# Performance work log

Hardware: AMD Instinct MI355X
Metric: run time of the kernel (lower is better)

Reference implementation:

```python
import jax, jax.numpy as jnp
import numpy as np

H = 8
DQ = 32
DK = 32
DV = 32
DC = DQ + DK  # concat dim for additive attention


def setup_inputs() -> dict:
    key = jax.random.key(0)
    ks = jax.random.split(key, 8)
    bs, Lq, Lk = 2, 384, 384
    q = jax.random.normal(ks[0], (bs, Lq, H * DQ), jnp.float32)
    k = jax.random.normal(ks[1], (bs, Lk, H * DK), jnp.float32)
    v = jax.random.normal(ks[2], (bs, Lk, H * DV), jnp.float32)
    q_sequence_lengths = jax.random.randint(ks[3], (bs,), 1, Lq + 1, dtype=jnp.int32)
    k_sequence_lengths = jax.random.randint(ks[4], (bs,), 1, Lk + 1, dtype=jnp.int32)
    bound = 1.0 / np.sqrt(DC)
    w1 = jax.random.uniform(ks[5], (H, DC, DC), jnp.float32, -bound, bound)
    b1 = jax.random.uniform(ks[6], (H, DC), jnp.float32, -bound, bound)
    w2 = jax.random.uniform(ks[7], (H, DC), jnp.float32, -1.0, 1.0)
    return {"q": q, "k": k, "v": v,
            "q_sequence_lengths": q_sequence_lengths,
            "k_sequence_lengths": k_sequence_lengths,
            "w1": w1, "b1": b1, "w2": w2}


def reference(q, k, v, q_sequence_lengths, k_sequence_lengths, w1, b1, w2):
    bs, Lq, _ = q.shape
    Lk = k.shape[1]
    # split heads: (b, h, L, d)
    qh = q.reshape(bs, Lq, H, DQ).transpose(0, 2, 1, 3)
    kh = k.reshape(bs, Lk, H, DK).transpose(0, 2, 1, 3)
    vh = v.reshape(bs, Lk, H, DV).transpose(0, 2, 1, 3)
    # additive scores: tanh(cat(q_i, k_j) @ W1 + b1) @ w2
    # cat @ W1 == q @ W1[:DQ] + k @ W1[DQ:]  (avoids materializing the cat)
    qW = jnp.einsum('bhqd,hde->bhqe', qh, w1[:, :DQ, :])
    kW = jnp.einsum('bhkd,hde->bhke', kh, w1[:, DQ:, :])
    hid = jnp.tanh(qW[:, :, :, None, :] + kW[:, :, None, :, :] + b1[None, :, None, None, :])  # (b,h,q,k,DC)
    scores = jnp.einsum('bhqke,he->bhqk', hid, w2)
    # key-side length mask (end padded)
    kmask = jnp.arange(Lk)[None, :] < k_sequence_lengths[:, None]  # (b, Lk)
    scores = jnp.where(kmask[:, None, None, :], scores, jnp.float32(-1e9))
    att = jax.nn.softmax(scores, axis=-1)  # (b,h,q,k)
    out = jnp.einsum('bhqk,bhkd->bqhd', att, vh)  # (b,q,h,DV)
    # query-side length mask zeros out padded query rows
    qmask = jnp.arange(Lq)[None, :] < q_sequence_lengths[:, None]  # (b, Lq)
    out = out * qmask[:, :, None, None].astype(out.dtype)
    return out.reshape(bs, Lq, H * DV), att
```

## Files before the change

kernel.cpp:

```cpp
#include <hip/hip_runtime.h>

#define NH 8
#define LQ 384
#define LK 384
#define BS 2

typedef float v4f __attribute__((ext_vector_type(4)));
__device__ __forceinline__ v4f fma4(v4f a, v4f b, v4f c) { return __builtin_elementwise_fma(a, b, c); }
__device__ __forceinline__ v4f sp4(float x) { v4f r; r.x = x; r.y = x; r.z = x; r.w = x; return r; }

__global__ __launch_bounds__(256) void pre_ek_kernel(
    const float* __restrict__ kin, const float* __restrict__ w1,
    const float* __restrict__ b1, float* __restrict__ ws)
{
    __shared__ float tile[16][65];
    const int bid = blockIdx.x;
    const int bh = bid / 24, kt = bid % 24;
    const int b = bh >> 3, h = bh & 7;
    const int k0 = kt * 16;
    const int tid = threadIdx.x;
    const int lane = tid & 63, w = tid >> 6;

    float w1c[32];
    const float* w1p = w1 + (size_t)(h * 64 + 32) * 64 + lane;
    #pragma unroll
    for (int d = 0; d < 32; ++d) w1c[d] = w1p[d * 64];
    const float bv = b1[h * 64 + lane];

    #pragma unroll
    for (int s = 0; s < 4; ++s) {
        int kr = w * 4 + s;
        const float* krow = kin + ((size_t)(b * LK + k0 + kr)) * (NH * 32) + h * 32;
        float acc = bv;
        #pragma unroll
        for (int d = 0; d < 32; ++d) acc = __builtin_fmaf(krow[d], w1c[d], acc);
        tile[kr][lane] = __expf(acc + acc);
    }
    __syncthreads();
    {
        int e4 = tid >> 4, k16 = tid & 15;
        float4 o;
        o.x = tile[k16][e4 * 4 + 0];
        o.y = tile[k16][e4 * 4 + 1];
        o.z = tile[k16][e4 * 4 + 2];
        o.w = tile[k16][e4 * 4 + 3];
        ((float4*)ws)[((size_t)(bh * 16 + e4)) * LK + k0 + k16] = o;
    }
}

__global__ __launch_bounds__(256) void attn_kernel(
    const float* __restrict__ qin, const float* __restrict__ vin,
    const int* __restrict__ qlens, const int* __restrict__ klens,
    const float* __restrict__ w1, const float* __restrict__ w2g,
    const float* __restrict__ ws,
    float* __restrict__ outg, float* __restrict__ attg)
{
    __shared__ __align__(16) float eqi_s[2][256];
    __shared__ __align__(16) float att_h[4][4 * 192];
    __shared__ __align__(16) float w2s[64];
    __shared__ float2 smu[2][4][2];
    __shared__ __align__(16) float4 pvp[2][2][4][8];

    const int tid = threadIdx.x, wave = tid >> 6, lane = tid & 63;
    const int pair = wave >> 1, hh = wave & 1;
    const int bh = blockIdx.x / 48, tile = blockIdx.x % 48;
    const int b = bh >> 3, h = bh & 7;
    const int q0 = tile * 8;
    const int klen = klens[b], qlen = qlens[b];

    {
        float w1c[32];
        const float* w1p = w1 + (size_t)h * 64 * 64 + lane;
        #pragma unroll
        for (int d = 0; d < 32; ++d) w1c[d] = w1p[d * 64];
        #pragma unroll
        for (int j = 0; j < 2; ++j) {
            int r = wave * 2 + j;
            const float* qp = qin + ((size_t)(b * LQ + q0 + r)) * (NH * 32) + h * 32;
            float a = 0.f;
            #pragma unroll
            for (int d = 0; d < 32; ++d) a = __builtin_fmaf(qp[d], w1c[d], a);
            eqi_s[r >> 2][lane * 4 + (r & 3)] = __expf(a + a);
        }
        if (wave == 0) w2s[lane] = w2g[h * 64 + lane];
    }
    __syncthreads();

    v4f sc[3];
    sc[0] = sp4(0.f); sc[1] = sp4(0.f); sc[2] = sp4(0.f);
    const float4* ekq = (const float4*)ws + ((size_t)bh * 16) * LK + hh * 192 + lane;
    const v4f*   eqp = (const v4f*)eqi_s[pair];
    const float4* w2p = (const float4*)w2s;

    float4 kva[3], kvb[3];
    #pragma unroll
    for (int c = 0; c < 3; ++c) kva[c] = ekq[c * 64];
    #pragma unroll
    for (int c = 0; c < 3; ++c) kvb[c] = ekq[LK + c * 64];

    #pragma unroll
    for (int e4 = 0; e4 < 16; ++e4) {
        float4* cur = (e4 & 1) ? kvb : kva;
        float4 kq0 = cur[0], kq1 = cur[1], kq2 = cur[2];
        if (e4 < 14) {
            const float4* np = ekq + (size_t)(e4 + 2) * LK;
            cur[0] = np[0]; cur[1] = np[64]; cur[2] = np[128];
        }
        v4f E0 = eqp[e4 * 4 + 0];
        v4f E1 = eqp[e4 * 4 + 1];
        v4f E2 = eqp[e4 * 4 + 2];
        v4f E3 = eqp[e4 * 4 + 3];
        float4 wv = w2p[e4];
        float4 kqs[3] = {kq0, kq1, kq2};
        #pragma unroll
        for (int c = 0; c < 3; ++c) {
            float4 kq = kqs[c];
            v4f t0 = fma4(E0, sp4(kq.x), sp4(1.f));
            v4f t1 = fma4(E1, sp4(kq.y), sp4(1.f));
            v4f t2 = fma4(E2, sp4(kq.z), sp4(1.f));
            v4f t3 = fma4(E3, sp4(kq.w), sp4(1.f));
            v4f p12 = t0 * t1, p34 = t2 * t3;
            v4f n12 = fma4(sp4(wv.y), t0, sp4(wv.x) * t1);
            v4f n34 = fma4(sp4(wv.w), t2, sp4(wv.z) * t3);
            v4f num = fma4(n34, p12, n12 * p34);
            v4f den = p12 * p34;
            v4f r;
            r.x = __builtin_amdgcn_rcpf(den.x);
            r.y = __builtin_amdgcn_rcpf(den.y);
            r.z = __builtin_amdgcn_rcpf(den.z);
            r.w = __builtin_amdgcn_rcpf(den.w);
            sc[c] = fma4(num, r, sc[c]);
        }
    }

    float s_[3][4];
    float m_[4] = {-3.4e38f, -3.4e38f, -3.4e38f, -3.4e38f};
    #pragma unroll
    for (int c = 0; c < 3; ++c) {
        int kk = hh * 192 + c * 64 + lane;
        bool ok = kk < klen;
        #pragma unroll
        for (int r = 0; r < 4; ++r) {
            s_[c][r] = ok ? -2.0f * sc[c][r] : -3.4e38f;
            m_[r] = fmaxf(m_[r], s_[c][r]);
        }
    }
    #pragma unroll
    for (int off = 32; off >= 1; off >>= 1) {
        #pragma unroll
        for (int r = 0; r < 4; ++r) m_[r] = fmaxf(m_[r], __shfl_xor(m_[r], off));
    }
    float e_[3][4];
    float u_[4] = {0.f, 0.f, 0.f, 0.f};
    #pragma unroll
    for (int c = 0; c < 3; ++c) {
        int kk = hh * 192 + c * 64 + lane;
        bool ok = kk < klen;
        #pragma unroll
        for (int r = 0; r < 4; ++r) {
            e_[c][r] = ok ? __expf(s_[c][r] - m_[r]) : 0.f;
            u_[r] += e_[c][r];
        }
    }
    #pragma unroll
    for (int off = 32; off >= 1; off >>= 1) {
        #pragma unroll
        for (int r = 0; r < 4; ++r) u_[r] += __shfl_xor(u_[r], off);
    }
    if (lane == 0) {
        #pragma unroll
        for (int r = 0; r < 4; ++r) smu[pair][r][hh] = make_float2(m_[r], u_[r]);
    }
    {
        float* ar = att_h[wave];
        #pragma unroll
        for (int c = 0; c < 3; ++c)
            #pragma unroll
            for (int r = 0; r < 4; ++r)
                ar[r * 192 + c * 64 + lane] = e_[c][r];
    }

    const int kf = lane >> 3, dg = lane & 7;
    const float* vbase = vin + (size_t)b * LK * (NH * 32) + h * 32
                       + (size_t)(hh * 192 + kf) * (NH * 32) + dg * 4;
    const float* ap = att_h[wave];
    float oa[4][4] = {{0.f,0.f,0.f,0.f},{0.f,0.f,0.f,0.f},{0.f,0.f,0.f,0.f},{0.f,0.f,0.f,0.f}};
    float4 vbuf[2];
    vbuf[0] = *(const float4*)(vbase);
    vbuf[1] = *(const float4*)(vbase + (size_t)8 * (NH * 32));
    #pragma unroll
    for (int i = 0; i < 24; ++i) {
        float4 vv = vbuf[i & 1];
        if (i < 22) vbuf[i & 1] = *(const float4*)(vbase + (size_t)((i + 2) * 8) * (NH * 32));
        int k0 = i * 8;
        #pragma unroll
        for (int r = 0; r < 4; ++r) {
            float a = ap[r * 192 + k0 + kf];
            oa[r][0] = __builtin_fmaf(a, vv.x, oa[r][0]);
            oa[r][1] = __builtin_fmaf(a, vv.y, oa[r][1]);
            oa[r][2] = __builtin_fmaf(a, vv.z, oa[r][2]);
            oa[r][3] = __builtin_fmaf(a, vv.w, oa[r][3]);
        }
    }
    #pragma unroll
    for (int r = 0; r < 4; ++r)
        #pragma unroll
        for (int u = 0; u < 4; ++u) {
            oa[r][u] += __shfl_xor(oa[r][u], 8);
            oa[r][u] += __shfl_xor(oa[r][u], 16);
            oa[r][u] += __shfl_xor(oa[r][u], 32);
        }
    __syncthreads();

    float f_[4];
    #pragma unroll
    for (int r = 0; r < 4; ++r) {
        float2 A = smu[pair][r][0], B = smu[pair][r][1];
        float mm = fmaxf(A.x, B.x);
        float uu = A.y * __expf(A.x - mm) + B.y * __expf(B.x - mm);
        f_[r] = __expf(m_[r] - mm) * __builtin_amdgcn_rcpf(uu);
    }

    if (kf == 0) {
        #pragma unroll
        for (int r = 0; r < 4; ++r)
            pvp[pair][hh][r][dg] = make_float4(oa[r][0] * f_[r], oa[r][1] * f_[r],
                                               oa[r][2] * f_[r], oa[r][3] * f_[r]);
    }
    __syncthreads();

    if (lane < 16) {
        int r = wave * 2 + (lane >> 3);
        int dgo = lane & 7;
        int q = q0 + r;
        float4 xa = pvp[r >> 2][0][r & 3][dgo];
        float4 xb = pvp[r >> 2][1][r & 3][dgo];
        float4 o4;
        bool ok = (q < qlen);
        o4.x = ok ? (xa.x + xb.x) : 0.f;
        o4.y = ok ? (xa.y + xb.y) : 0.f;
        o4.z = ok ? (xa.z + xb.z) : 0.f;
        o4.w = ok ? (xa.w + xb.w) : 0.f;
        ((float4*)(outg + ((size_t)(b * LQ + q)) * (NH * 32) + h * 32))[dgo] = o4;
    }

    {
        float* ag = attg + ((size_t)(bh * LQ + q0 + pair * 4)) * LK + hh * 192;
        #pragma unroll
        for (int r = 0; r < 4; ++r) {
            #pragma unroll
            for (int c = 0; c < 3; ++c) ag[c * 64 + lane] = e_[c][r] * f_[r];
            ag += LK;
        }
    }
}

extern "C" void kernel_launch(void* const* d_in, const int* in_sizes, int n_in,
                              void* d_out, int out_size, void* d_ws, size_t ws_size,
                              hipStream_t stream) {
    const float* q    = (const float*)d_in[0];
    const float* k    = (const float*)d_in[1];
    const float* v    = (const float*)d_in[2];
    const int*   qlen = (const int*)d_in[3];
    const int*   klen = (const int*)d_in[4];
    const float* w1   = (const float*)d_in[5];
    const float* b1   = (const float*)d_in[6];
    const float* w2   = (const float*)d_in[7];
    float* out = (float*)d_out;
    float* att = out + (size_t)BS * LQ * NH * 32;
    float* ws  = (float*)d_ws;

    pre_ek_kernel<<<384, 256, 0, stream>>>(k, w1, b1, ws);
    attn_kernel<<<768, 256, 0, stream>>>(q, v, qlen, klen, w1, w2, ws, out, att);
}
```

Measured before the change: 94.54 us.

## Repartition attention block to six waves each owning 64 keys for all 8 queries

The attention kernel moves from 4 waves (2 query groups × 2 key halves of 192) to 6 waves, each handling 64 keys for all 8 query rows with 8-wide vector math. Each ws key-feature load is now reused across 8 queries instead of 4, which cuts global reads of the precomputed key exponentials and shortens the per-thread serial loop. Softmax statistics and partial PV results are combined across 6 waves through shared memory, and the attention writes move before the final barrier. The cost is more threads per block, more registers for 8-row accumulators, and a heavier cross-wave reduction.

```diff
diff --git a/kernel.cpp b/kernel.cpp
--- a/kernel.cpp
+++ b/kernel.cpp
@@ -5,9 +5,9 @@
 #define LK 384
 #define BS 2
 
-typedef float v4f __attribute__((ext_vector_type(4)));
-__device__ __forceinline__ v4f fma4(v4f a, v4f b, v4f c) { return __builtin_elementwise_fma(a, b, c); }
-__device__ __forceinline__ v4f sp4(float x) { v4f r; r.x = x; r.y = x; r.z = x; r.w = x; return r; }
+typedef float v8f __attribute__((ext_vector_type(8)));
+__device__ __forceinline__ v8f fma8(v8f a, v8f b, v8f c) { return __builtin_elementwise_fma(a, b, c); }
+__device__ __forceinline__ v8f sp8(float x) { v8f r = {x, x, x, x, x, x, x, x}; return r; }
 
 __global__ __launch_bounds__(256) void pre_ek_kernel(
     const float* __restrict__ kin, const float* __restrict__ w1,
@@ -48,27 +48,26 @@
     }
 }
 
-__global__ __launch_bounds__(256) void attn_kernel(
+__global__ __launch_bounds__(384) void attn_kernel(
     const float* __restrict__ qin, const float* __restrict__ vin,
     const int* __restrict__ qlens, const int* __restrict__ klens,
     const float* __restrict__ w1, const float* __restrict__ w2g,
     const float* __restrict__ ws,
     float* __restrict__ outg, float* __restrict__ attg)
 {
-    __shared__ __align__(16) float eqi_s[2][256];
-    __shared__ __align__(16) float att_h[4][4 * 192];
+    __shared__ __align__(32) float eqi_s[8 * 64];
+    __shared__ __align__(16) float att_h[6][512];
     __shared__ __align__(16) float w2s[64];
-    __shared__ float2 smu[2][4][2];
-    __shared__ __align__(16) float4 pvp[2][2][4][8];
+    __shared__ float2 smu[6][8];
+    __shared__ __align__(16) float4 pvp[6][8][8];
 
     const int tid = threadIdx.x, wave = tid >> 6, lane = tid & 63;
-    const int pair = wave >> 1, hh = wave & 1;
     const int bh = blockIdx.x / 48, tile = blockIdx.x % 48;
     const int b = bh >> 3, h = bh & 7;
     const int q0 = tile * 8;
     const int klen = klens[b], qlen = qlens[b];
 
-    {
+    if (wave < 4) {
         float w1c[32];
         const float* w1p = w1 + (size_t)h * 64 * 64 + lane;
         #pragma unroll
@@ -80,122 +79,98 @@
             float a = 0.f;
             #pragma unroll
             for (int d = 0; d < 32; ++d) a = __builtin_fmaf(qp[d], w1c[d], a);
-            eqi_s[r >> 2][lane * 4 + (r & 3)] = __expf(a + a);
-        }
-        if (wave == 0) w2s[lane] = w2g[h * 64 + lane];
-    }
-    __syncthreads();
-
-    v4f sc[3];
-    sc[0] = sp4(0.f); sc[1] = sp4(0.f); sc[2] = sp4(0.f);
-    const float4* ekq = (const float4*)ws + ((size_t)bh * 16) * LK + hh * 192 + lane;
-    const v4f*   eqp = (const v4f*)eqi_s[pair];
+            eqi_s[lane * 8 + r] = __expf(a + a);
+        }
+    } else if (wave == 4) {
+        w2s[lane] = w2g[h * 64 + lane];
+    }
+    __syncthreads();
+
+    v8f sc = sp8(0.f);
+    const float4* ekp = (const float4*)ws + ((size_t)bh * 16) * LK + wave * 64 + lane;
+    const v8f* eqv = (const v8f*)eqi_s;
     const float4* w2p = (const float4*)w2s;
 
-    float4 kva[3], kvb[3];
-    #pragma unroll
-    for (int c = 0; c < 3; ++c) kva[c] = ekq[c * 64];
-    #pragma unroll
-    for (int c = 0; c < 3; ++c) kvb[c] = ekq[LK + c * 64];
-
+    float4 kva = ekp[0];
+    float4 kvb = ekp[LK];
     #pragma unroll
     for (int e4 = 0; e4 < 16; ++e4) {
-        float4* cur = (e4 & 1) ? kvb : kva;
-        float4 kq0 = cur[0], kq1 = cur[1], kq2 = cur[2];
+        float4 kq = (e4 & 1) ? kvb : kva;
         if (e4 < 14) {
-            const float4* np = ekq + (size_t)(e4 + 2) * LK;
-            cur[0] = np[0]; cur[1] = np[64]; cur[2] = np[128];
-        }
-        v4f E0 = eqp[e4 * 4 + 0];
-        v4f E1 = eqp[e4 * 4 + 1];
-        v4f E2 = eqp[e4 * 4 + 2];
-        v4f E3 = eqp[e4 * 4 + 3];
+            float4 nx = ekp[(size_t)(e4 + 2) * LK];
+            if (e4 & 1) kvb = nx; else kva = nx;
+        }
+        v8f E0 = eqv[e4 * 4 + 0];
+        v8f E1 = eqv[e4 * 4 + 1];
+        v8f E2 = eqv[e4 * 4 + 2];
+        v8f E3 = eqv[e4 * 4 + 3];
         float4 wv = w2p[e4];
-        float4 kqs[3] = {kq0, kq1, kq2};
-        #pragma unroll
-        for (int c = 0; c < 3; ++c) {
-            float4 kq = kqs[c];
-            v4f t0 = fma4(E0, sp4(kq.x), sp4(1.f));
-            v4f t1 = fma4(E1, sp4(kq.y), sp4(1.f));
-            v4f t2 = fma4(E2, sp4(kq.z), sp4(1.f));
-            v4f t3 = fma4(E3, sp4(kq.w), sp4(1.f));
-            v4f p12 = t0 * t1, p34 = t2 * t3;
-            v4f n12 = fma4(sp4(wv.y), t0, sp4(wv.x) * t1);
-            v4f n34 = fma4(sp4(wv.w), t2, sp4(wv.z) * t3);
-            v4f num = fma4(n34, p12, n12 * p34);
-            v4f den = p12 * p34;
-            v4f r;
-            r.x = __builtin_amdgcn_rcpf(den.x);
-            r.y = __builtin_amdgcn_rcpf(den.y);
-            r.z = __builtin_amdgcn_rcpf(den.z);
-            r.w = __builtin_amdgcn_rcpf(den.w);
-            sc[c] = fma4(num, r, sc[c]);
-        }
-    }
-
-    float s_[3][4];
-    float m_[4] = {-3.4e38f, -3.4e38f, -3.4e38f, -3.4e38f};
-    #pragma unroll
-    for (int c = 0; c < 3; ++c) {
-        int kk = hh * 192 + c * 64 + lane;
-        bool ok = kk < klen;
-        #pragma unroll
-        for (int r = 0; r < 4; ++r) {
-            s_[c][r] = ok ? -2.0f * sc[c][r] : -3.4e38f;
-            m_[r] = fmaxf(m_[r], s_[c][r]);
-        }
-    }
-    #pragma unroll
-    for (int off = 32; off >= 1; off >>= 1) {
-        #pragma unroll
-        for (int r = 0; r < 4; ++r) m_[r] = fmaxf(m_[r], __shfl_xor(m_[r], off));
-    }
-    float e_[3][4];
-    float u_[4] = {0.f, 0.f, 0.f, 0.f};
-    #pragma unroll
-    for (int c = 0; c < 3; ++c) {
-        int kk = hh * 192 + c * 64 + lane;
-        bool ok = kk < klen;
-        #pragma unroll
-        for (int r = 0; r < 4; ++r) {
-            e_[c][r] = ok ? __expf(s_[c][r] - m_[r]) : 0.f;
-            u_[r] += e_[c][r];
-        }
-    }
-    #pragma unroll
-    for (int off = 32; off >= 1; off >>= 1) {
-        #pragma unroll
-        for (int r = 0; r < 4; ++r) u_[r] += __shfl_xor(u_[r], off);
-    }
+        v8f t0 = fma8(E0, sp8(kq.x), sp8(1.f));
+        v8f t1 = fma8(E1, sp8(kq.y), sp8(1.f));
+        v8f t2 = fma8(E2, sp8(kq.z), sp8(1.f));
+        v8f t3 = fma8(E3, sp8(kq.w), sp8(1.f));
+        v8f p12 = t0 * t1, p34 = t2 * t3;
+        v8f n12 = fma8(sp8(wv.y), t0, sp8(wv.x) * t1);
+        v8f n34 = fma8(sp8(wv.w), t2, sp8(wv.z) * t3);
+        v8f num = fma8(n34, p12, n12 * p34);
+        v8f den = p12 * p34;
+        v8f rr;
+        #pragma unroll
+        for (int j = 0; j < 8; ++j) rr[j] = __builtin_amdgcn_rcpf(den[j]);
+        sc = fma8(num, rr, sc);
+    }
+
+    const int kk = wave * 64 + lane;
+    const bool ok = kk < klen;
+    float s_[8], m_[8];
+    #pragma unroll
+    for (int r = 0; r < 8; ++r) {
+        s_[r] = ok ? -2.0f * sc[r] : -3.4e38f;
+        m_[r] = s_[r];
+    }
+    #pragma unroll
+    for (int off = 32; off >= 1; off >>= 1)
+        #pragma unroll
+        for (int r = 0; r < 8; ++r) m_[r] = fmaxf(m_[r], __shfl_xor(m_[r], off));
+    float e_[8], u_[8];
+    #pragma unroll
+    for (int r = 0; r < 8; ++r) {
+        e_[r] = ok ? __expf(s_[r] - m_[r]) : 0.f;
+        u_[r] = e_[r];
+    }
+    #pragma unroll
+    for (int off = 32; off >= 1; off >>= 1)
+        #pragma unroll
+        for (int r = 0; r < 8; ++r) u_[r] += __shfl_xor(u_[r], off);
     if (lane == 0) {
         #pragma unroll
-        for (int r = 0; r < 4; ++r) smu[pair][r][hh] = make_float2(m_[r], u_[r]);
+        for (int r = 0; r < 8; ++r) smu[wave][r] = make_float2(m_[r], u_[r]);
     }
     {
         float* ar = att_h[wave];
         #pragma unroll
-        for (int c = 0; c < 3; ++c)
-            #pragma unroll
-            for (int r = 0; r < 4; ++r)
-                ar[r * 192 + c * 64 + lane] = e_[c][r];
+        for (int r = 0; r < 8; ++r) ar[r * 64 + lane] = e_[r];
     }
 
     const int kf = lane >> 3, dg = lane & 7;
     const float* vbase = vin + (size_t)b * LK * (NH * 32) + h * 32
-                       + (size_t)(hh * 192 + kf) * (NH * 32) + dg * 4;
+                       + (size_t)(wave * 64 + kf) * (NH * 32) + dg * 4;
     const float* ap = att_h[wave];
-    float oa[4][4] = {{0.f,0.f,0.f,0.f},{0.f,0.f,0.f,0.f},{0.f,0.f,0.f,0.f},{0.f,0.f,0.f,0.f}};
-    float4 vbuf[2];
-    vbuf[0] = *(const float4*)(vbase);
-    vbuf[1] = *(const float4*)(vbase + (size_t)8 * (NH * 32));
-    #pragma unroll
-    for (int i = 0; i < 24; ++i) {
-        float4 vv = vbuf[i & 1];
-        if (i < 22) vbuf[i & 1] = *(const float4*)(vbase + (size_t)((i + 2) * 8) * (NH * 32));
+    float oa[8][4] = {{0.f,0.f,0.f,0.f},{0.f,0.f,0.f,0.f},{0.f,0.f,0.f,0.f},{0.f,0.f,0.f,0.f},
+                      {0.f,0.f,0.f,0.f},{0.f,0.f,0.f,0.f},{0.f,0.f,0.f,0.f},{0.f,0.f,0.f,0.f}};
+    float4 vbuf0 = *(const float4*)(vbase);
+    float4 vbuf1 = *(const float4*)(vbase + (size_t)8 * (NH * 32));
+    #pragma unroll
+    for (int i = 0; i < 8; ++i) {
+        float4 vv = (i & 1) ? vbuf1 : vbuf0;
+        if (i < 6) {
+            float4 nx = *(const float4*)(vbase + (size_t)((i + 2) * 8) * (NH * 32));
+            if (i & 1) vbuf1 = nx; else vbuf0 = nx;
+        }
         int k0 = i * 8;
         #pragma unroll
-        for (int r = 0; r < 4; ++r) {
-            float a = ap[r * 192 + k0 + kf];
+        for (int r = 0; r < 8; ++r) {
+            float a = ap[r * 64 + k0 + kf];
             oa[r][0] = __builtin_fmaf(a, vv.x, oa[r][0]);
             oa[r][1] = __builtin_fmaf(a, vv.y, oa[r][1]);
             oa[r][2] = __builtin_fmaf(a, vv.z, oa[r][2]);
@@ -203,7 +178,7 @@
         }
     }
     #pragma unroll
-    for (int r = 0; r < 4; ++r)
+    for (int r = 0; r < 8; ++r)
         #pragma unroll
         for (int u = 0; u < 4; ++u) {
             oa[r][u] += __shfl_xor(oa[r][u], 8);
@@ -212,46 +187,44 @@
         }
     __syncthreads();
 
-    float f_[4];
-    #pragma unroll
-    for (int r = 0; r < 4; ++r) {
-        float2 A = smu[pair][r][0], B = smu[pair][r][1];
-        float mm = fmaxf(A.x, B.x);
-        float uu = A.y * __expf(A.x - mm) + B.y * __expf(B.x - mm);
+    float f_[8];
+    #pragma unroll
+    for (int r = 0; r < 8; ++r) {
+        float2 p0 = smu[0][r], p1 = smu[1][r], p2 = smu[2][r];
+        float2 p3 = smu[3][r], p4 = smu[4][r], p5 = smu[5][r];
+        float mm = fmaxf(fmaxf(fmaxf(p0.x, p1.x), fmaxf(p2.x, p3.x)), fmaxf(p4.x, p5.x));
+        float uu = p0.y * __expf(p0.x - mm) + p1.y * __expf(p1.x - mm)
+                 + p2.y * __expf(p2.x - mm) + p3.y * __expf(p3.x - mm)
+                 + p4.y * __expf(p4.x - mm) + p5.y * __expf(p5.x - mm);
         f_[r] = __expf(m_[r] - mm) * __builtin_amdgcn_rcpf(uu);
     }
 
     if (kf == 0) {
         #pragma unroll
-        for (int r = 0; r < 4; ++r)
-            pvp[pair][hh][r][dg] = make_float4(oa[r][0] * f_[r], oa[r][1] * f_[r],
-                                               oa[r][2] * f_[r], oa[r][3] * f_[r]);
-    }
-    __syncthreads();
-
-    if (lane < 16) {
-        int r = wave * 2 + (lane >> 3);
-        int dgo = lane & 7;
+        for (int r = 0; r < 8; ++r)
+            pvp[wave][r][dg] = make_float4(oa[r][0] * f_[r], oa[r][1] * f_[r],
+                                           oa[r][2] * f_[r], oa[r][3] * f_[r]);
+    }
+
+    {
+        float* ag = attg + ((size_t)(bh * LQ + q0)) * LK + wave * 64 + lane;
+        #pragma unroll
+        for (int r = 0; r < 8; ++r) ag[(size_t)r * LK] = e_[r] * f_[r];
+    }
+    __syncthreads();
+
+    if (wave == 0) {
+        int r = lane >> 3, dgo = lane & 7;
+        float4 x0 = pvp[0][r][dgo], x1 = pvp[1][r][dgo], x2 = pvp[2][r][dgo];
+        float4 x3 = pvp[3][r][dgo], x4 = pvp[4][r][dgo], x5 = pvp[5][r][dgo];
         int q = q0 + r;
-        float4 xa = pvp[r >> 2][0][r & 3][dgo];
-        float4 xb = pvp[r >> 2][1][r & 3][dgo];
+        bool okq = (q < qlen);
         float4 o4;
-        bool ok = (q < qlen);
-        o4.x = ok ? (xa.x + xb.x) : 0.f;
-        o4.y = ok ? (xa.y + xb.y) : 0.f;
-        o4.z = ok ? (xa.z + xb.z) : 0.f;
-        o4.w = ok ? (xa.w + xb.w) : 0.f;
+        o4.x = okq ? (x0.x + x1.x + x2.x + x3.x + x4.x + x5.x) : 0.f;
+        o4.y = okq ? (x0.y + x1.y + x2.y + x3.y + x4.y + x5.y) : 0.f;
+        o4.z = okq ? (x0.z + x1.z + x2.z + x3.z + x4.z + x5.z) : 0.f;
+        o4.w = okq ? (x0.w + x1.w + x2.w + x3.w + x4.w + x5.w) : 0.f;
         ((float4*)(outg + ((size_t)(b * LQ + q)) * (NH * 32) + h * 32))[dgo] = o4;
-    }
-
-    {
-        float* ag = attg + ((size_t)(bh * LQ + q0 + pair * 4)) * LK + hh * 192;
-        #pragma unroll
-        for (int r = 0; r < 4; ++r) {
-            #pragma unroll
-            for (int c = 0; c < 3; ++c) ag[c * 64 + lane] = e_[c][r] * f_[r];
-            ag += LK;
-        }
     }
 }
 
@@ -271,5 +244,5 @@
     float* ws  = (float*)d_ws;
 
     pre_ek_kernel<<<384, 256, 0, stream>>>(k, w1, b1, ws);
-    attn_kernel<<<768, 256, 0, stream>>>(q, v, qlen, klen, w1, w2, ws, out, att);
+    attn_kernel<<<768, 384, 0, stream>>>(q, v, qlen, klen, w1, w2, ws, out, att);
 }
```

New measurement: 105.4 us. 11.5% more time.
